# Optimization experiments

Hardware: AMD Instinct MI355X
Metric: run time of the kernel (lower is better)

The kernel has to match this reference:

```python
import jax, jax.numpy as jnp
import numpy as np


def squash(s):
    # s: (..., d); v = ||s|| / (1 + ||s||^2) * s
    norm = jnp.linalg.norm(s, axis=-1, keepdims=True)
    return norm / (1.0 + norm * norm) * s


def setup_inputs() -> dict:
    key = jax.random.key(0)
    k1, k2, k3 = jax.random.split(key, 3)
    batch, n_in, d_in, n_out, d_out = 256, 1152, 8, 10, 16
    u_i = jax.random.normal(k1, (batch, n_in, d_in), dtype=jnp.float32)
    weight = jax.random.normal(k2, (1, n_in, n_out, d_in, d_out), dtype=jnp.float32)
    bias = jax.random.normal(k3, (n_in, n_out, 1), dtype=jnp.float32)
    return {"u_i": u_i, "weight": weight, "bias": bias, "r": 3}


def reference(u_i, weight, bias, r):
    batch, n_in, d_in = u_i.shape
    # predictions u_j|i: (batch, n_in, n_out, d_out)
    u_ji = jnp.einsum('bnd,node->bnoe', u_i, weight[0]) + bias  # bias (n_in,n_out,1) broadcasts over d_out
    # dynamic routing
    b = jnp.zeros(u_ji.shape[:3], dtype=u_ji.dtype)  # (batch, n_in, n_out)
    v = None
    for _ in range(r):  # r is a small static iteration count
        c = jax.nn.softmax(b, axis=-1)                      # over n_out
        s = jnp.einsum('bno,bnoe->boe', c, u_ji)            # weighted sum over n_in
        v = squash(s)                                       # (batch, n_out, d_out)
        b = b + jnp.einsum('bnoe,boe->bno', u_ji, v)        # agreement update
    return v
```

## Files before the change

kernel.cpp:

```cpp
#include <hip/hip_runtime.h>


#define B    256
#define N    1152
#define NO   10
#define DI   8
#define DE   16
#define NTILE   8
#define NTILES  144
#define BG      64
#define BGS     4
#define THREADS 320
#define WFLT    (NO * DI * DE)
#define WTILE   (NTILE * WFLT)

#define SP_OFF 0
#define SP_SZ  (NTILES * B * NO * DE)
#define VS_OFF (SP_OFF + SP_SZ)
#define VS_SZ  (B * NO * DE)

__global__ __launch_bounds__(THREADS, 3)
void routing_kernel(const float* __restrict__ u,
                    const float* __restrict__ w,
                    const float* __restrict__ bias,
                    const float* __restrict__ vsum,
                    float* __restrict__ s_part,
                    const int has_v) {
    __shared__ __align__(16) float lds_w[WTILE];
    __shared__ float lgx[2][NO][BG];
    const int tid  = threadIdx.x;
    const int lane = tid & 63;
    const int wv   = __builtin_amdgcn_readfirstlane(tid >> 6);
    const int o0   = wv * 2;
    const int b    = blockIdx.y * BG + lane;
    const int n0   = blockIdx.x * NTILE;

    {
        const float4* src = (const float4*)(w + (size_t)n0 * WFLT);
        float4* dst = (float4*)lds_w;
#pragma unroll
        for (int j = 0; j < 8; ++j)
            dst[tid + j * THREADS] = src[tid + j * THREADS];
    }

    float4 vv[2][4];
#pragma unroll
    for (int oi = 0; oi < 2; ++oi)
#pragma unroll
        for (int eq = 0; eq < 4; ++eq)
            vv[oi][eq] = make_float4(0.f, 0.f, 0.f, 0.f);
    if (has_v) {
#pragma unroll
        for (int oi = 0; oi < 2; ++oi)
#pragma unroll
            for (int eq = 0; eq < 4; ++eq)
                vv[oi][eq] = *(const float4*)(vsum + ((size_t)b * NO + o0 + oi) * DE + eq * 4);
    }

    float4 acc[2][4];
#pragma unroll
    for (int oi = 0; oi < 2; ++oi)
#pragma unroll
        for (int eq = 0; eq < 4; ++eq)
            acc[oi][eq] = make_float4(0.f, 0.f, 0.f, 0.f);

    __syncthreads();

    for (int i = 0; i < NTILE; ++i) {
        const int n = n0 + i;

        const float* up = u + ((size_t)b * N + n) * DI;
        const float4 u0 = *(const float4*)up;
        const float4 u1 = *(const float4*)(up + 4);
        const float ur[DI] = {u0.x, u0.y, u0.z, u0.w, u1.x, u1.y, u1.z, u1.w};

        const float* wp = lds_w + i * WFLT + o0 * (DI * DE);
        float4 uji[2][4];
#pragma unroll
        for (int oi = 0; oi < 2; ++oi) {
            const float bv = bias[n * NO + o0 + oi];
#pragma unroll
            for (int eq = 0; eq < 4; ++eq)
                uji[oi][eq] = make_float4(bv, bv, bv, bv);
#pragma unroll
            for (int d = 0; d < DI; ++d) {
                const float* wrow = wp + oi * (DI * DE) + d * DE;
#pragma unroll
                for (int eq = 0; eq < 4; ++eq) {
                    const float4 w4 = *(const float4*)(wrow + eq * 4);
                    uji[oi][eq].x += ur[d] * w4.x;
                    uji[oi][eq].y += ur[d] * w4.y;
                    uji[oi][eq].z += ur[d] * w4.z;
                    uji[oi][eq].w += ur[d] * w4.w;
                }
            }
        }

        float c[2];
        if (has_v) {
            const int buf = i & 1;
#pragma unroll
            for (int oi = 0; oi < 2; ++oi) {
                float lg = 0.f;
#pragma unroll
                for (int eq = 0; eq < 4; ++eq)
                    lg += uji[oi][eq].x * vv[oi][eq].x + uji[oi][eq].y * vv[oi][eq].y
                        + uji[oi][eq].z * vv[oi][eq].z + uji[oi][eq].w * vv[oi][eq].w;
                lgx[buf][o0 + oi][lane] = lg;
            }
            __syncthreads();
            float l[NO];
#pragma unroll
            for (int o = 0; o < NO; ++o) l[o] = lgx[buf][o][lane];

            float m = l[0];
#pragma unroll
            for (int o = 1; o < NO; ++o) m = fmaxf(m, l[o]);
            float sum = 0.f;
#pragma unroll
            for (int o = 0; o < NO; ++o) { l[o] = __expf(l[o] - m); sum += l[o]; }
            const float inv = 1.f / sum;
            c[0] = l[o0] * inv;
            c[1] = l[o0 + 1] * inv;
        } else {
            c[0] = 0.1f; c[1] = 0.1f;
        }

#pragma unroll
        for (int oi = 0; oi < 2; ++oi)
#pragma unroll
            for (int eq = 0; eq < 4; ++eq) {
                acc[oi][eq].x += c[oi] * uji[oi][eq].x;
                acc[oi][eq].y += c[oi] * uji[oi][eq].y;
                acc[oi][eq].z += c[oi] * uji[oi][eq].z;
                acc[oi][eq].w += c[oi] * uji[oi][eq].w;
            }
    }

    float* sp = s_part + (((size_t)blockIdx.x * B + b) * NO + o0) * DE;
#pragma unroll
    for (int oi = 0; oi < 2; ++oi)
#pragma unroll
        for (int eq = 0; eq < 4; ++eq)
            *(float4*)(sp + oi * DE + eq * 4) = acc[oi][eq];
}

__global__ __launch_bounds__(256)
void squash_kernel(const float* __restrict__ s_part,
                   float* __restrict__ vsum,
                   float* __restrict__ out,
                   const int accum) {
    __shared__ __align__(16) float4 part[4][64];
    const int tid  = threadIdx.x;
    const int lane = tid & 63;
    const int q    = tid >> 6;
    const int f4   = blockIdx.x * 64 + lane;

    const float4* sp = (const float4*)s_part + (size_t)(q * 36) * (B * NO * DE / 4) + f4;
    float4 s = make_float4(0.f, 0.f, 0.f, 0.f);
#pragma unroll 12
    for (int i = 0; i < 36; ++i) {
        const float4 t = sp[(size_t)i * (B * NO * DE / 4)];
        s.x += t.x; s.y += t.y; s.z += t.z; s.w += t.w;
    }
    part[q][lane] = s;
    __syncthreads();

    if (q == 0) {
#pragma unroll
        for (int j = 1; j < 4; ++j) {
            const float4 t = part[j][lane];
            s.x += t.x; s.y += t.y; s.z += t.z; s.w += t.w;
        }
        float nsq = s.x * s.x + s.y * s.y + s.z * s.z + s.w * s.w;
        nsq += __shfl_xor(nsq, 1);
        nsq += __shfl_xor(nsq, 2);
        const float nrm   = sqrtf(nsq);
        const float scale = nrm / (1.f + nsq);
        const float4 val = make_float4(s.x * scale, s.y * scale,
                                       s.z * scale, s.w * scale);
        ((float4*)out)[f4] = val;
        float4* vp = (float4*)vsum + f4;
        if (accum) {
            const float4 old = *vp;
            *vp = make_float4(old.x + val.x, old.y + val.y,
                              old.z + val.z, old.w + val.w);
        } else {
            *vp = val;
        }
    }
}

extern "C" void kernel_launch(void* const* d_in, const int* in_sizes, int n_in,
                              void* d_out, int out_size, void* d_ws, size_t ws_size,
                              hipStream_t stream) {
    const float* u    = (const float*)d_in[0];
    const float* w    = (const float*)d_in[1];
    const float* bias = (const float*)d_in[2];

    float* wsf    = (float*)d_ws;
    float* s_part = wsf + SP_OFF;
    float* vsum   = wsf + VS_OFF;
    float* out    = (float*)d_out;

    for (int it = 0; it < 3; ++it) {
        routing_kernel<<<dim3(NTILES, BGS), THREADS, 0, stream>>>(
            u, w, bias, vsum, s_part, it > 0);
        squash_kernel<<<(B * NO * DE / 4) / 64, 256, 0, stream>>>(
            s_part, vsum, out, it > 0);
    }
}
```

Measured before the change: 218.7 us.

## Read routing weights directly from global memory and shrink input tiles to four

Removes the LDS staging of the weight tile and its barrier, so each wave reads its weight slice straight from global memory (wave-uniform addresses, served by cache). When the workspace is large enough it also halves the n-tile size to 4 and doubles the grid to 288x4 blocks, raising parallelism. The reduction kernel now takes a runtime tile count, which makes the partial-sum array twice as large and the squash pass read twice as much data. Its loop is no longer fixed-unrolled.

```diff
diff --git a/kernel.cpp b/kernel.cpp
--- a/kernel.cpp
+++ b/kernel.cpp
@@ -6,19 +6,12 @@
 #define NO   10
 #define DI   8
 #define DE   16
-#define NTILE   8
-#define NTILES  144
 #define BG      64
 #define BGS     4
 #define THREADS 320
-#define WFLT    (NO * DI * DE)
-#define WTILE   (NTILE * WFLT)
-
-#define SP_OFF 0
-#define SP_SZ  (NTILES * B * NO * DE)
-#define VS_OFF (SP_OFF + SP_SZ)
-#define VS_SZ  (B * NO * DE)
-
+#define SPSTRIDE (B * NO * DE)
+
+template <int NTILE_T>
 __global__ __launch_bounds__(THREADS, 3)
 void routing_kernel(const float* __restrict__ u,
                     const float* __restrict__ w,
@@ -26,22 +19,13 @@
                     const float* __restrict__ vsum,
                     float* __restrict__ s_part,
                     const int has_v) {
-    __shared__ __align__(16) float lds_w[WTILE];
     __shared__ float lgx[2][NO][BG];
     const int tid  = threadIdx.x;
     const int lane = tid & 63;
     const int wv   = __builtin_amdgcn_readfirstlane(tid >> 6);
     const int o0   = wv * 2;
     const int b    = blockIdx.y * BG + lane;
-    const int n0   = blockIdx.x * NTILE;
-
-    {
-        const float4* src = (const float4*)(w + (size_t)n0 * WFLT);
-        float4* dst = (float4*)lds_w;
-#pragma unroll
-        for (int j = 0; j < 8; ++j)
-            dst[tid + j * THREADS] = src[tid + j * THREADS];
-    }
+    const int n0   = blockIdx.x * NTILE_T;
 
     float4 vv[2][4];
 #pragma unroll
@@ -64,9 +48,7 @@
         for (int eq = 0; eq < 4; ++eq)
             acc[oi][eq] = make_float4(0.f, 0.f, 0.f, 0.f);
 
-    __syncthreads();
-
-    for (int i = 0; i < NTILE; ++i) {
+    for (int i = 0; i < NTILE_T; ++i) {
         const int n = n0 + i;
 
         const float* up = u + ((size_t)b * N + n) * DI;
@@ -74,7 +56,7 @@
         const float4 u1 = *(const float4*)(up + 4);
         const float ur[DI] = {u0.x, u0.y, u0.z, u0.w, u1.x, u1.y, u1.z, u1.w};
 
-        const float* wp = lds_w + i * WFLT + o0 * (DI * DE);
+        const float* wp = w + ((size_t)n * NO + o0) * (DI * DE);
         float4 uji[2][4];
 #pragma unroll
         for (int oi = 0; oi < 2; ++oi) {
@@ -149,6 +131,7 @@
 void squash_kernel(const float* __restrict__ s_part,
                    float* __restrict__ vsum,
                    float* __restrict__ out,
+                   const int tpw,
                    const int accum) {
     __shared__ __align__(16) float4 part[4][64];
     const int tid  = threadIdx.x;
@@ -156,11 +139,10 @@
     const int q    = tid >> 6;
     const int f4   = blockIdx.x * 64 + lane;
 
-    const float4* sp = (const float4*)s_part + (size_t)(q * 36) * (B * NO * DE / 4) + f4;
+    const float4* sp = (const float4*)s_part + (size_t)(q * tpw) * (SPSTRIDE / 4) + f4;
     float4 s = make_float4(0.f, 0.f, 0.f, 0.f);
-#pragma unroll 12
-    for (int i = 0; i < 36; ++i) {
-        const float4 t = sp[(size_t)i * (B * NO * DE / 4)];
+    for (int i = 0; i < tpw; ++i) {
+        const float4 t = sp[(size_t)i * (SPSTRIDE / 4)];
         s.x += t.x; s.y += t.y; s.z += t.z; s.w += t.w;
     }
     part[q][lane] = s;
@@ -198,15 +180,21 @@
     const float* w    = (const float*)d_in[1];
     const float* bias = (const float*)d_in[2];
 
+    const size_t need4 = ((size_t)(N / 4) * SPSTRIDE + SPSTRIDE) * sizeof(float);
+    const bool   big   = ws_size >= need4;
+    const int    ntiles = big ? (N / 4) : (N / 8);
+
     float* wsf    = (float*)d_ws;
-    float* s_part = wsf + SP_OFF;
-    float* vsum   = wsf + VS_OFF;
+    float* s_part = wsf;
+    float* vsum   = wsf + (size_t)ntiles * SPSTRIDE;
     float* out    = (float*)d_out;
 
+    const dim3 rgrid(ntiles, BGS), rblk(THREADS);
     for (int it = 0; it < 3; ++it) {
-        routing_kernel<<<dim3(NTILES, BGS), THREADS, 0, stream>>>(
-            u, w, bias, vsum, s_part, it > 0);
-        squash_kernel<<<(B * NO * DE / 4) / 64, 256, 0, stream>>>(
-            s_part, vsum, out, it > 0);
+        if (big)
+            routing_kernel<4><<<rgrid, rblk, 0, stream>>>(u, w, bias, vsum, s_part, it > 0);
+        else
+            routing_kernel<8><<<rgrid, rblk, 0, stream>>>(u, w, bias, vsum, s_part, it > 0);
+        squash_kernel<<<160, 256, 0, stream>>>(s_part, vsum, out, ntiles / 4, it > 0);
     }
 }
```

After: 248.4 us. 1.14x slower.
